# Optimization experiments

Hardware: AMD Instinct MI355X
Metric: run time of the kernel (lower is better)

Reference implementation:

```python
import jax, jax.numpy as jnp
import numpy as np

NHEADS = 16
DIM = 1024


def setup_inputs() -> dict:
    key = jax.random.key(0)
    k1, k2, k3 = jax.random.split(key, 3)
    B, S, D = 4, 2048, DIM
    x = jax.random.normal(k1, (B, S, D), dtype=jnp.float32)
    W_qkv = jax.random.normal(k2, (D, 3 * D), dtype=jnp.float32) * (1.0 / np.sqrt(D))
    b_qkv = jax.random.normal(k3, (3 * D,), dtype=jnp.float32) * 0.01
    return {"x": x, "W_qkv": W_qkv, "b_qkv": b_qkv}


def reference(x, W_qkv, b_qkv):
    B, S, D = x.shape
    H = NHEADS
    Dh = D // H
    qkv = x @ W_qkv + b_qkv                      # [B, S, 3D]
    q, k, v = jnp.split(qkv, 3, axis=-1)         # each [B, S, D]
    # [B, S, H, Dh] -> [B, H, S, Dh]
    q = q.reshape(B, S, H, Dh).transpose(0, 2, 1, 3)
    k = k.reshape(B, S, H, Dh).transpose(0, 2, 1, 3)
    v = v.reshape(B, S, H, Dh).transpose(0, 2, 1, 3)
    scale = 1.0 / np.sqrt(Dh).astype(np.float32)
    scores = jnp.einsum('bhqd,bhkd->bhqk', q, k) * scale
    attn = jax.nn.softmax(scores, axis=-1)
    out = jnp.einsum('bhqk,bhkd->bhqd', attn, v)  # [B, H, S, Dh]
    # FAITHFUL to original: raw view [B,H,S,Dh] -> [B, S, H*Dh] (no transpose back)
    return out.reshape(B, S, H * Dh)
```

## Files before the change

### kernel.cpp

```cpp
#include <hip/hip_runtime.h>
#include <hip/hip_bf16.h>
#include <stdint.h>

typedef float          f32x4  __attribute__((ext_vector_type(4)));
typedef float          f32x16 __attribute__((ext_vector_type(16)));
typedef short          s16x8  __attribute__((ext_vector_type(8)));
typedef unsigned short u16;
typedef u16            u16x4 __attribute__((ext_vector_type(4)));
typedef u16            u16x8 __attribute__((ext_vector_type(8)));
typedef unsigned int   u32;
typedef u32            u32x4 __attribute__((ext_vector_type(4)));

#define DMODEL 1024
#define NH     16
#define DH     64
#define SEQ    2048
#define BATCH  4
#define NROW   (BATCH*SEQ)
#define N3     (3*DMODEL)

#define KEXP 0.1803368801f

__device__ __forceinline__ u16 f2bf(float f) {
    __hip_bfloat16 h = __float2bfloat16(f);
    u16 u;
    __builtin_memcpy(&u, &h, 2);
    return u;
}

typedef const __attribute__((address_space(1))) void* gas_t;
typedef __attribute__((address_space(3))) void* las_t;
__device__ __forceinline__ void async16(void* lds, const void* g) {
    __builtin_amdgcn_global_load_lds((gas_t)g, (las_t)lds, 16, 0, 0);
}

__device__ __forceinline__ f32x4 mfma16(s16x8 a, s16x8 b, f32x4 c) {
    return __builtin_amdgcn_mfma_f32_16x16x32_bf16(a, b, c, 0, 0, 0);
}
__device__ __forceinline__ f32x16 mfma32(s16x8 a, s16x8 b, f32x16 c) {
    return __builtin_amdgcn_mfma_f32_32x32x16_bf16(a, b, c, 0, 0, 0);
}

#define SWZ(row) (((row) & 7) ^ ((((row) >> 3) & 3) << 1))

__global__ __launch_bounds__(256)
void cast_fused_kernel(const float* __restrict__ xin, u16* __restrict__ xb,
                       const float* __restrict__ W,  u16* __restrict__ Wt)
{
    __shared__ u16 T[64][72];
    const int t = threadIdx.x;
    if (blockIdx.x < 4096) {
        const int i = blockIdx.x * 256 + t;
        const f32x4* p = (const f32x4*)xin;
        f32x4 a = p[2*i], b = p[2*i+1];
        u16x8 o;
        o[0]=f2bf(a[0]); o[1]=f2bf(a[1]); o[2]=f2bf(a[2]); o[3]=f2bf(a[3]);
        o[4]=f2bf(b[0]); o[5]=f2bf(b[1]); o[6]=f2bf(b[2]); o[7]=f2bf(b[3]);
        ((u16x8*)xb)[i] = o;
        return;
    }
    const int bid2 = blockIdx.x - 4096;
    const int n0 = (bid2 % (N3/64)) * 64;
    const int k0 = (bid2 / (N3/64)) * 64;
    {
        const int c4 = t & 15, rr = t >> 4;
        #pragma unroll
        for (int ri = 0; ri < 4; ++ri) {
            const int r = ri*16 + rr;
            f32x4 v = *(const f32x4*)&W[(size_t)(k0 + r) * N3 + n0 + c4*4];
            #pragma unroll
            for (int e = 0; e < 4; ++e) T[r][c4*4+e] = f2bf(v[e]);
        }
    }
    __syncthreads();
    {
        const int nr = t >> 2, kq = t & 3;
        #pragma unroll
        for (int pp = 0; pp < 2; ++pp) {
            const int kb = kq + pp*4;
            u16x8 o;
            #pragma unroll
            for (int e = 0; e < 8; ++e) o[e] = T[kb*8+e][nr];
            *(u16x8*)&Wt[(size_t)(n0 + nr) * DMODEL + k0 + kb*8] = o;
        }
    }
}

__global__ __launch_bounds__(256)
void qkv_mfma_kernel(const u16* __restrict__ xb, const u16* __restrict__ Wt,
                     const float* __restrict__ bias,
                     u16* __restrict__ Qb, u16* __restrict__ Kb, u16* __restrict__ Vt)
{
    __shared__ u16 As[128*32];
    __shared__ u16 Bs[128*32];

    const int tid  = threadIdx.x;
    const int lane = tid & 63;
    const int w    = tid >> 6;
    const int wm   = w >> 1, wn = w & 1;
    const int n0   = blockIdx.x * 128;
    const int m0   = blockIdx.y * 128;

    const int srow = w*32 + (lane >> 2);
    const int scol = (lane & 3) * 8;
    u16* ad0 = &As[(w*2+0)*512 + lane*8];
    u16* ad1 = &As[(w*2+1)*512 + lane*8];
    u16* bd0 = &Bs[(w*2+0)*512 + lane*8];
    u16* bd1 = &Bs[(w*2+1)*512 + lane*8];
    const u16* ag0 = &xb[(size_t)(m0 + srow)      * DMODEL + scol];
    const u16* ag1 = &xb[(size_t)(m0 + srow + 16) * DMODEL + scol];
    const u16* bg0 = &Wt[(size_t)(n0 + srow)      * DMODEL + scol];
    const u16* bg1 = &Wt[(size_t)(n0 + srow + 16) * DMODEL + scol];

    f32x4 acc[4][4];
    #pragma unroll
    for (int i = 0; i < 4; ++i)
        #pragma unroll
        for (int j = 0; j < 4; ++j)
            acc[i][j] = (f32x4){0.f, 0.f, 0.f, 0.f};

    for (int k0 = 0; k0 < DMODEL; k0 += 32) {
        async16(ad0, ag0 + k0);
        async16(ad1, ag1 + k0);
        async16(bd0, bg0 + k0);
        async16(bd1, bg1 + k0);
        __syncthreads();
        s16x8 af[4], bf[4];
        #pragma unroll
        for (int mi = 0; mi < 4; ++mi)
            af[mi] = *(const s16x8*)&As[(wm*64 + mi*16 + (lane&15))*32 + (lane>>4)*8];
        #pragma unroll
        for (int ni = 0; ni < 4; ++ni)
            bf[ni] = *(const s16x8*)&Bs[(wn*64 + ni*16 + (lane&15))*32 + (lane>>4)*8];
        #pragma unroll
        for (int mi = 0; mi < 4; ++mi)
            #pragma unroll
            for (int ni = 0; ni < 4; ++ni)
                acc[mi][ni] = mfma16(af[mi], bf[ni], acc[mi][ni]);
        __syncthreads();
    }

    const int part  = n0 >> 10;
    const int col_l = lane & 15;
    const int h     = ((n0 & 1023) >> 6) + wn;
    float bv[4];
    #pragma unroll
    for (int ni = 0; ni < 4; ++ni) bv[ni] = bias[n0 + wn*64 + ni*16 + col_l];

    const int rbase = m0 + wm*64 + (lane>>4)*4;
    u16* qk = (part == 0) ? Qb : Kb;
    #pragma unroll
    for (int mi = 0; mi < 4; ++mi) {
        const int r0 = rbase + mi*16;
        const int b  = r0 >> 11;
        const int s  = r0 & 2047;
        #pragma unroll
        for (int ni = 0; ni < 4; ++ni) {
            const int d = ni*16 + col_l;
            if (part < 2) {
                u16* base = &qk[(((size_t)b*NH + h)*SEQ + s)*DH + d];
                #pragma unroll
                for (int j = 0; j < 4; ++j) {
                    float v = acc[mi][ni][j] + bv[ni];
                    if (part == 0) v *= KEXP;
                    base[(size_t)j*DH] = f2bf(v);
                }
            } else {
                u16x4 o;
                #pragma unroll
                for (int j = 0; j < 4; ++j) o[j] = f2bf(acc[mi][ni][j] + bv[ni]);
                *(u16x4*)&Vt[(((size_t)b*NH + h)*DH + d)*SEQ + s] = o;
            }
        }
    }
}

__global__ __launch_bounds__(512)
void attn_mfma_kernel(const u16* __restrict__ Qb, const u16* __restrict__ Kb,
                      const u16* __restrict__ Vt, float* __restrict__ out)
{
    __shared__ u16 Ks[2][2][64*64];
    __shared__ u16 Vs[2][2][64*64];

    const int tid  = threadIdx.x;
    const int lane = tid & 63;
    const int w    = tid >> 6;
    const int q0   = blockIdx.x * 256;
    const int bh   = blockIdx.y;
    const size_t qkoff = (size_t)bh * SEQ * DH;

    const int l5  = lane >> 5;
    const int l31 = lane & 31;

    s16x8 qf[4];
    {
        const u16* qp = &Qb[qkoff + (size_t)(q0 + w*32 + l31)*DH];
        #pragma unroll
        for (int dop = 0; dop < 4; ++dop)
            qf[dop] = *(const s16x8*)(qp + dop*16 + l5*8);
    }

    const int skey = tid >> 3;
    const int sg   = tid & 7;
    const int gsw8 = (sg ^ SWZ(skey)) * 8;
    const int sdo  = tid * 8;
    const u16* kgb = &Kb[qkoff + (size_t)skey * DH + gsw8];
    const u16* vgb = &Vt[((size_t)bh * DH + skey) * SEQ + gsw8];

    f32x16 oacc[2];
    #pragma unroll
    for (int i = 0; i < 16; ++i) { oacc[0][i] = 0.f; oacc[1][i] = 0.f; }
    float psum = 0.f;

#define STAGE(buf, kb2) do {                                          \
        const size_t _o = (size_t)(kb2) * 128;                        \
        async16(&Ks[buf][0][sdo], kgb + (_o     ) * DH);              \
        async16(&Ks[buf][1][sdo], kgb + (_o + 64) * DH);              \
        async16(&Vs[buf][0][sdo], vgb + _o);                          \
        async16(&Vs[buf][1][sdo], vgb + _o + 64);                     \
    } while (0)

#define COMPUTE(buf, sub) do {                                                   \
        const char* ksb = (const char*)Ks[buf][sub];                             \
        const char* vsb = (const char*)Vs[buf][sub];                             \
        f32x16 sacc[2];                                                          \
        _Pragma("unroll")                                                        \
        for (int i = 0; i < 16; ++i) { sacc[0][i] = 0.f; sacc[1][i] = 0.f; }     \
        _Pragma("unroll")                                                        \
        for (int dop = 0; dop < 4; ++dop) {                                      \
            _Pragma("unroll")                                                    \
            for (int kb32 = 0; kb32 < 2; ++kb32) {                               \
                const int rowK = kb32*32 + l31;                                  \
                const int gK   = 2*dop + l5;                                     \
                s16x8 kf = *(const s16x8*)(ksb + rowK*128                        \
                                           + ((gK ^ SWZ(rowK)) << 4));           \
                sacc[kb32] = mfma32(kf, qf[dop], sacc[kb32]);                    \
            }                                                                    \
        }                                                                        \
            \
                                      \
        u32 pk2[2][8];                                                           \
        float rs = 0.f;                                                          \
        _Pragma("unroll")                                                        \
        for (int kb32 = 0; kb32 < 2; ++kb32) {                                   \
            _Pragma("unroll")                                                    \
            for (int pj = 0; pj < 8; ++pj) {                                     \
                const int r0 = 4*(pj>>1) + 2*(pj&1);                             \
                const float p0 = __builtin_amdgcn_exp2f(sacc[kb32][r0]);         \
                const float p1 = __builtin_amdgcn_exp2f(sacc[kb32][r0+1]);       \
                rs += p0 + p1;                                                   \
                pk2[kb32][pj] = (u32)f2bf(p0) | ((u32)f2bf(p1) << 16);           \
            }                                                                    \
        }                                                                        \
        psum += rs;                                                              \
              \
                    \
        _Pragma("unroll")                                                        \
        for (int kop = 0; kop < 4; ++kop) {                                      \
            const int kb = kop >> 1;                                             \
            const int k2 = (kop & 1) * 4;                                        \
            const u32 s0 = l5 ? pk2[kb][k2+0] : pk2[kb][k2+2];                   \
            const u32 s1 = l5 ? pk2[kb][k2+1] : pk2[kb][k2+3];                   \
            const u32 f0 = __shfl_xor(s0, 32);                                   \
            const u32 f1 = __shfl_xor(s1, 32);                                   \
            u32x4 pw;                                                            \
            pw[0] = l5 ? f0 : pk2[kb][k2+0];                                     \
            pw[1] = l5 ? f1 : pk2[kb][k2+1];                                     \
            pw[2] = l5 ? pk2[kb][k2+2] : f0;                                     \
            pw[3] = l5 ? pk2[kb][k2+3] : f1;                                     \
            s16x8 paf;                                                           \
            __builtin_memcpy(&paf, &pw, 16);                                     \
            _Pragma("unroll")                                                    \
            for (int ndblk = 0; ndblk < 2; ++ndblk) {                            \
                const int rowV = ndblk*32 + l31;                                 \
                const int gV   = 2*kop + l5;                                     \
                s16x8 vf = *(const s16x8*)(vsb + rowV*128                        \
                                           + ((gV ^ SWZ(rowV)) << 4));           \
                oacc[ndblk] = mfma32(paf, vf, oacc[ndblk]);                      \
            }                                                                    \
        }                                                                        \
    } while (0)

    STAGE(0, 0);
    asm volatile("s_waitcnt vmcnt(0)" ::: "memory");
    __builtin_amdgcn_s_barrier();

    for (int kb2 = 0; kb2 < SEQ/128; kb2 += 2) {
        STAGE(1, kb2 + 1);
        COMPUTE(0, 0);
        COMPUTE(0, 1);
        asm volatile("s_waitcnt vmcnt(0)" ::: "memory");
        __builtin_amdgcn_s_barrier();
        if (kb2 + 2 < SEQ/128) STAGE(0, kb2 + 2);
        COMPUTE(1, 0);
        COMPUTE(1, 1);
        asm volatile("s_waitcnt vmcnt(0)" ::: "memory");
        __builtin_amdgcn_s_barrier();
    }

#undef STAGE
#undef COMPUTE

    const float pt = psum + __shfl_xor(psum, 32);
    const float rinv_own = 1.0f / pt;
    float* op = out + qkoff;
    #pragma unroll
    for (int r = 0; r < 16; ++r) {
        const int qrow = (r & 3) + 8*(r >> 2) + 4*l5;
        const float ri = __shfl(rinv_own, qrow);
        const size_t q = (size_t)(q0 + w*32 + qrow);
        op[q*DH + l31]      = oacc[0][r] * ri;
        op[q*DH + 32 + l31] = oacc[1][r] * ri;
    }
}

extern "C" void kernel_launch(void* const* d_in, const int* in_sizes, int n_in,
                              void* d_out, int out_size, void* d_ws, size_t ws_size,
                              hipStream_t stream)
{
    const float* x    = (const float*)d_in[0];
    const float* W    = (const float*)d_in[1];
    const float* bias = (const float*)d_in[2];
    float* out = (float*)d_out;

    u16* xb = (u16*)d_ws;
    u16* Wt = xb + (size_t)NROW * DMODEL;
    u16* Qb = Wt + (size_t)N3 * DMODEL;
    u16* Kb = Qb + (size_t)BATCH*NH*SEQ*DH;
    u16* Vt = Kb + (size_t)BATCH*NH*SEQ*DH;

    cast_fused_kernel<<<4096 + 768, 256, 0, stream>>>(x, xb, W, Wt);
    qkv_mfma_kernel<<<dim3(N3/128, NROW/128), 256, 0, stream>>>(xb, Wt, bias, Qb, Kb, Vt);
    attn_mfma_kernel<<<dim3(SEQ/256, BATCH*NH), 512, 0, stream>>>(Qb, Kb, Vt, out);
}
```

Measured before the change: 170.9 us.

## Process two 32-row query tiles per wave in attention kernel

Each wave now handles 64 query rows (two 32-row MFMA tiles) instead of 32, so each block covers 512 queries and the grid halves. K and V fragments loaded from shared memory are reused across both query tiles, halving LDS reads and global K/V staging per query. The cost is doubled accumulator registers, which may lower occupancy. The grid also shrinks to 256 blocks on a 256-CU device, leaving one block per CU.

```diff
diff --git a/kernel.cpp b/kernel.cpp
--- a/kernel.cpp
+++ b/kernel.cpp
@@ -185,19 +185,20 @@
     const int tid  = threadIdx.x;
     const int lane = tid & 63;
     const int w    = tid >> 6;
-    const int q0   = blockIdx.x * 256;
+    const int q0   = blockIdx.x * 512;
     const int bh   = blockIdx.y;
     const size_t qkoff = (size_t)bh * SEQ * DH;
 
     const int l5  = lane >> 5;
     const int l31 = lane & 31;
 
-    s16x8 qf[4];
-    {
-        const u16* qp = &Qb[qkoff + (size_t)(q0 + w*32 + l31)*DH];
+    s16x8 qf[2][4];
+    #pragma unroll
+    for (int mi = 0; mi < 2; ++mi) {
+        const u16* qp = &Qb[qkoff + (size_t)(q0 + w*64 + mi*32 + l31)*DH];
         #pragma unroll
         for (int dop = 0; dop < 4; ++dop)
-            qf[dop] = *(const s16x8*)(qp + dop*16 + l5*8);
+            qf[mi][dop] = *(const s16x8*)(qp + dop*16 + l5*8);
     }
 
     const int skey = tid >> 3;
@@ -207,10 +208,12 @@
     const u16* kgb = &Kb[qkoff + (size_t)skey * DH + gsw8];
     const u16* vgb = &Vt[((size_t)bh * DH + skey) * SEQ + gsw8];
 
-    f32x16 oacc[2];
-    #pragma unroll
-    for (int i = 0; i < 16; ++i) { oacc[0][i] = 0.f; oacc[1][i] = 0.f; }
-    float psum = 0.f;
+    f32x16 oacc[2][2];
+    #pragma unroll
+    for (int mi = 0; mi < 2; ++mi)
+        #pragma unroll
+        for (int i = 0; i < 16; ++i) { oacc[mi][0][i] = 0.f; oacc[mi][1][i] = 0.f; }
+    float psum[2] = {0.f, 0.f};
 
 #define STAGE(buf, kb2) do {                                          \
         const size_t _o = (size_t)(kb2) * 128;                        \
@@ -223,9 +226,11 @@
 #define COMPUTE(buf, sub) do {                                                   \
         const char* ksb = (const char*)Ks[buf][sub];                             \
         const char* vsb = (const char*)Vs[buf][sub];                             \
-        f32x16 sacc[2];                                                          \
+        f32x16 sacc[2][2];                                                       \
         _Pragma("unroll")                                                        \
-        for (int i = 0; i < 16; ++i) { sacc[0][i] = 0.f; sacc[1][i] = 0.f; }     \
+        for (int mi = 0; mi < 2; ++mi)                                           \
+            _Pragma("unroll")                                                    \
+            for (int i = 0; i < 16; ++i) { sacc[mi][0][i] = 0.f; sacc[mi][1][i] = 0.f; } \
         _Pragma("unroll")                                                        \
         for (int dop = 0; dop < 4; ++dop) {                                      \
             _Pragma("unroll")                                                    \
@@ -234,49 +239,53 @@
                 const int gK   = 2*dop + l5;                                     \
                 s16x8 kf = *(const s16x8*)(ksb + rowK*128                        \
                                            + ((gK ^ SWZ(rowK)) << 4));           \
-                sacc[kb32] = mfma32(kf, qf[dop], sacc[kb32]);                    \
+                _Pragma("unroll")                                                \
+                for (int mi = 0; mi < 2; ++mi)                                   \
+                    sacc[mi][kb32] = mfma32(kf, qf[mi][dop], sacc[mi][kb32]);    \
             }                                                                    \
         }                                                                        \
-            \
-                                      \
-        u32 pk2[2][8];                                                           \
-        float rs = 0.f;                                                          \
+                 \
+        u32 pk2[2][2][8];                                                        \
         _Pragma("unroll")                                                        \
-        for (int kb32 = 0; kb32 < 2; ++kb32) {                                   \
+        for (int mi = 0; mi < 2; ++mi) {                                         \
+            float rs = 0.f;                                                      \
             _Pragma("unroll")                                                    \
-            for (int pj = 0; pj < 8; ++pj) {                                     \
-                const int r0 = 4*(pj>>1) + 2*(pj&1);                             \
-                const float p0 = __builtin_amdgcn_exp2f(sacc[kb32][r0]);         \
-                const float p1 = __builtin_amdgcn_exp2f(sacc[kb32][r0+1]);       \
-                rs += p0 + p1;                                                   \
-                pk2[kb32][pj] = (u32)f2bf(p0) | ((u32)f2bf(p1) << 16);           \
+            for (int kb32 = 0; kb32 < 2; ++kb32) {                               \
+                _Pragma("unroll")                                                \
+                for (int pj = 0; pj < 8; ++pj) {                                 \
+                    const int r0 = 4*(pj>>1) + 2*(pj&1);                         \
+                    const float p0 = __builtin_amdgcn_exp2f(sacc[mi][kb32][r0]); \
+                    const float p1 = __builtin_amdgcn_exp2f(sacc[mi][kb32][r0+1]); \
+                    rs += p0 + p1;                                               \
+                    pk2[mi][kb32][pj] = (u32)f2bf(p0) | ((u32)f2bf(p1) << 16);   \
+                }                                                                \
             }                                                                    \
+            psum[mi] += rs;                                                      \
         }                                                                        \
-        psum += rs;                                                              \
-              \
-                    \
+               \
         _Pragma("unroll")                                                        \
         for (int kop = 0; kop < 4; ++kop) {                                      \
             const int kb = kop >> 1;                                             \
             const int k2 = (kop & 1) * 4;                                        \
-            const u32 s0 = l5 ? pk2[kb][k2+0] : pk2[kb][k2+2];                   \
-            const u32 s1 = l5 ? pk2[kb][k2+1] : pk2[kb][k2+3];                   \
-            const u32 f0 = __shfl_xor(s0, 32);                                   \
-            const u32 f1 = __shfl_xor(s1, 32);                                   \
-            u32x4 pw;                                                            \
-            pw[0] = l5 ? f0 : pk2[kb][k2+0];                                     \
-            pw[1] = l5 ? f1 : pk2[kb][k2+1];                                     \
-            pw[2] = l5 ? pk2[kb][k2+2] : f0;                                     \
-            pw[3] = l5 ? pk2[kb][k2+3] : f1;                                     \
-            s16x8 paf;                                                           \
-            __builtin_memcpy(&paf, &pw, 16);                                     \
+            const int gV = 2*kop + l5;                                           \
+            const int rowV0 = l31, rowV1 = 32 + l31;                             \
+            s16x8 vf0 = *(const s16x8*)(vsb + rowV0*128 + ((gV ^ SWZ(rowV0)) << 4)); \
+            s16x8 vf1 = *(const s16x8*)(vsb + rowV1*128 + ((gV ^ SWZ(rowV1)) << 4)); \
             _Pragma("unroll")                                                    \
-            for (int ndblk = 0; ndblk < 2; ++ndblk) {                            \
-                const int rowV = ndblk*32 + l31;                                 \
-                const int gV   = 2*kop + l5;                                     \
-                s16x8 vf = *(const s16x8*)(vsb + rowV*128                        \
-                                           + ((gV ^ SWZ(rowV)) << 4));           \
-                oacc[ndblk] = mfma32(paf, vf, oacc[ndblk]);                      \
+            for (int mi = 0; mi < 2; ++mi) {                                     \
+                const u32 s0 = l5 ? pk2[mi][kb][k2+0] : pk2[mi][kb][k2+2];       \
+                const u32 s1 = l5 ? pk2[mi][kb][k2+1] : pk2[mi][kb][k2+3];       \
+                const u32 f0 = __shfl_xor(s0, 32);                               \
+                const u32 f1 = __shfl_xor(s1, 32);                               \
+                u32x4 pw;                                                        \
+                pw[0] = l5 ? f0 : pk2[mi][kb][k2+0];                             \
+                pw[1] = l5 ? f1 : pk2[mi][kb][k2+1];                             \
+                pw[2] = l5 ? pk2[mi][kb][k2+2] : f0;                             \
+                pw[3] = l5 ? pk2[mi][kb][k2+3] : f1;                             \
+                s16x8 paf;                                                       \
+                __builtin_memcpy(&paf, &pw, 16);                                 \
+                oacc[mi][0] = mfma32(paf, vf0, oacc[mi][0]);                     \
+                oacc[mi][1] = mfma32(paf, vf1, oacc[mi][1]);                     \
             }                                                                    \
         }                                                                        \
     } while (0)
@@ -301,16 +310,19 @@
 #undef STAGE
 #undef COMPUTE
 
-    const float pt = psum + __shfl_xor(psum, 32);
-    const float rinv_own = 1.0f / pt;
     float* op = out + qkoff;
     #pragma unroll
-    for (int r = 0; r < 16; ++r) {
-        const int qrow = (r & 3) + 8*(r >> 2) + 4*l5;
-        const float ri = __shfl(rinv_own, qrow);
-        const size_t q = (size_t)(q0 + w*32 + qrow);
-        op[q*DH + l31]      = oacc[0][r] * ri;
-        op[q*DH + 32 + l31] = oacc[1][r] * ri;
+    for (int mi = 0; mi < 2; ++mi) {
+        const float pt = psum[mi] + __shfl_xor(psum[mi], 32);
+        const float rinv_own = 1.0f / pt;
+        #pragma unroll
+        for (int r = 0; r < 16; ++r) {
+            const int qrow = (r & 3) + 8*(r >> 2) + 4*l5;
+            const float ri = __shfl(rinv_own, qrow);
+            const size_t q = (size_t)(q0 + w*64 + mi*32 + qrow);
+            op[q*DH + l31]      = oacc[mi][0][r] * ri;
+            op[q*DH + 32 + l31] = oacc[mi][1][r] * ri;
+        }
     }
 }
 
@@ -331,5 +343,5 @@
 
     cast_fused_kernel<<<4096 + 768, 256, 0, stream>>>(x, xb, W, Wt);
     qkv_mfma_kernel<<<dim3(N3/128, NROW/128), 256, 0, stream>>>(xb, Wt, bias, Qb, Kb, Vt);
-    attn_mfma_kernel<<<dim3(SEQ/256, BATCH*NH), 512, 0, stream>>>(Qb, Kb, Vt, out);
-}
+    attn_mfma_kernel<<<dim3(SEQ/512, BATCH*NH), 512, 0, stream>>>(Qb, Kb, Vt, out);
+}
```

Measured after the change: 172.9 us. Within noise of the previous version (+1.1%).
